# Kernel optimization log

Measured on AMD Instinct MI355X. Metric: run time of the kernel, lower is better.

## Reference

```python
import jax, jax.numpy as jnp
import numpy as np

B, OBS_LEN, IN_DIM, H, PRED_LEN = 32768, 8, 2, 128, 12
PRIOR_STD = 0.1
DROPOUT = 0.1


def _uni(k, shape, fan):
    b = 1.0 / np.sqrt(fan)
    return jax.random.uniform(k, shape, jnp.float32, -b, b)


def setup_inputs() -> dict:
    key = jax.random.key(0)
    ks = jax.random.split(key, 16)
    inp = {"obs_seq": jax.random.normal(ks[0], (B, OBS_LEN, IN_DIM), jnp.float32)}
    # encoder nn.LSTM params (torch init: U(-1/sqrt(H), 1/sqrt(H)))
    inp["enc_wih0"] = _uni(ks[1], (4 * H, IN_DIM), H)
    inp["enc_whh0"] = _uni(ks[2], (4 * H, H), H)
    inp["enc_bih0"] = _uni(ks[3], (4 * H,), H)
    inp["enc_bhh0"] = _uni(ks[4], (4 * H,), H)
    inp["enc_wih1"] = _uni(ks[5], (4 * H, H), H)
    inp["enc_whh1"] = _uni(ks[6], (4 * H, H), H)
    inp["enc_bih1"] = _uni(ks[7], (4 * H,), H)
    inp["enc_bhh1"] = _uni(ks[8], (4 * H,), H)
    # Bayesian decoder cell: kaiming_uniform(a=sqrt(5)) -> U(-1/sqrt(fan_in), 1/sqrt(fan_in))
    inp["din_wmu"] = _uni(ks[9], (4 * H, IN_DIM), IN_DIM)
    inp["din_wrho"] = jnp.full((4 * H, IN_DIM), -3.0, jnp.float32)
    inp["din_bmu"] = jnp.zeros((4 * H,), jnp.float32)
    inp["din_brho"] = jnp.full((4 * H,), -3.0, jnp.float32)
    inp["dhid_wmu"] = _uni(ks[10], (4 * H, H), H)
    inp["dhid_wrho"] = jnp.full((4 * H, H), -3.0, jnp.float32)
    inp["dhid_bmu"] = jnp.zeros((4 * H,), jnp.float32)
    inp["dhid_brho"] = jnp.full((4 * H,), -3.0, jnp.float32)
    # Bayesian output layer hidden -> 4
    inp["out_wmu"] = _uni(ks[11], (4, H), H)
    inp["out_wrho"] = jnp.full((4, H), -3.0, jnp.float32)
    inp["out_bmu"] = jnp.zeros((4,), jnp.float32)
    inp["out_brho"] = jnp.full((4,), -3.0, jnp.float32)
    return inp


def _lstm_layer(xs, wih, whh, bih, bhh):
    # xs: (B, T, D). PyTorch gate order: i, f, g, o.
    h0 = jnp.zeros((xs.shape[0], H), xs.dtype)
    bias = bih + bhh

    def step(carry, xt):
        h, c = carry
        g = xt @ wih.T + h @ whh.T + bias
        i, f, gg, o = jnp.split(g, 4, axis=-1)
        c = jax.nn.sigmoid(f) * c + jax.nn.sigmoid(i) * jnp.tanh(gg)
        h = jax.nn.sigmoid(o) * jnp.tanh(c)
        return (h, c), h

    (h, c), hs = jax.lax.scan(step, (h0, h0), jnp.swapaxes(xs, 0, 1))
    return jnp.swapaxes(hs, 0, 1), (h, c)


def _kl(mu, rho):
    # KL(N(mu, std^2) || N(0, PRIOR_STD^2)), std = softplus(rho)
    std = jax.nn.softplus(rho)
    return jnp.sum(jnp.log(PRIOR_STD / std) + (std * std + mu * mu) / (2.0 * PRIOR_STD * PRIOR_STD) - 0.5)


def _forward(obs_seq, enc_wih0, enc_whh0, enc_bih0, enc_bhh0,
             enc_wih1, enc_whh1, enc_bih1, enc_bhh1,
             din_wmu, din_wrho, din_bmu, din_brho,
             dhid_wmu, dhid_wrho, dhid_bmu, dhid_brho,
             out_wmu, out_wrho, out_bmu, out_brho):
    # ---- encoder (training mode: inter-layer dropout) ----
    hs0, _ = _lstm_layer(obs_seq, enc_wih0, enc_whh0, enc_bih0, enc_bhh0)
    keep = jax.random.bernoulli(jax.random.key(1), 1.0 - DROPOUT, hs0.shape)
    hs0 = jnp.where(keep, hs0 / (1.0 - DROPOUT), 0.0)
    _, (h, c) = _lstm_layer(hs0, enc_wih1, enc_whh1, enc_bih1, enc_bhh1)

    # ---- variational decoder: resample Bayesian weights every step ----
    din_wstd = jax.nn.softplus(din_wrho)
    din_bstd = jax.nn.softplus(din_brho)
    dhid_wstd = jax.nn.softplus(dhid_wrho)
    dhid_bstd = jax.nn.softplus(dhid_brho)
    out_wstd = jax.nn.softplus(out_wrho)
    out_bstd = jax.nn.softplus(out_brho)

    step_keys = jax.random.split(jax.random.key(2), PRED_LEN)

    def dstep(carry, k):
        h, c, x = carry
        k1, k2, k3, k4, k5, k6 = jax.random.split(k, 6)
        w_in = din_wmu + din_wstd * jax.random.normal(k1, din_wmu.shape, jnp.float32)
        b_in = din_bmu + din_bstd * jax.random.normal(k2, din_bmu.shape, jnp.float32)
        w_hid = dhid_wmu + dhid_wstd * jax.random.normal(k3, dhid_wmu.shape, jnp.float32)
        b_hid = dhid_bmu + dhid_bstd * jax.random.normal(k4, dhid_bmu.shape, jnp.float32)
        w_out = out_wmu + out_wstd * jax.random.normal(k5, out_wmu.shape, jnp.float32)
        b_out = out_bmu + out_bstd * jax.random.normal(k6, out_bmu.shape, jnp.float32)
        g = x @ w_in.T + h @ w_hid.T + (b_in + b_hid)
        i, f, gg, o = jnp.split(g, 4, axis=-1)
        c_new = jax.nn.sigmoid(f) * c + jax.nn.sigmoid(i) * jnp.tanh(gg)
        h_new = jax.nn.sigmoid(o) * jnp.tanh(c_new)
        out = h_new @ w_out.T + b_out
        mu_xy = out[:, :2]
        log_sigma = jnp.clip(out[:, 2:], -4.0, 2.0)
        return (h_new, c_new, mu_xy), (mu_xy, log_sigma)

    _, (mus, lss) = jax.lax.scan(dstep, (h, c, obs_seq[:, -1, :]), step_keys)
    mu = jnp.swapaxes(mus, 0, 1)        # (B, pred_len, 2)
    log_sigma = jnp.swapaxes(lss, 0, 1)  # (B, pred_len, 2)

    # KL is overwritten each step; since std/mu are eps-independent it equals the analytic sum
    kl = (_kl(din_wmu, din_wrho) + _kl(din_bmu, din_brho)
          + _kl(dhid_wmu, dhid_wrho) + _kl(dhid_bmu, dhid_brho)
          + _kl(out_wmu, out_wrho) + _kl(out_bmu, out_brho))
    return mu, log_sigma, kl


def reference(obs_seq, enc_wih0, enc_whh0, enc_bih0, enc_bhh0,
              enc_wih1, enc_whh1, enc_bih1, enc_bhh1,
              din_wmu, din_wrho, din_bmu, din_brho,
              dhid_wmu, dhid_wrho, dhid_bmu, dhid_brho,
              out_wmu, out_wrho, out_bmu, out_brho):
    return _forward(obs_seq, enc_wih0, enc_whh0, enc_bih0, enc_bhh0,
                    enc_wih1, enc_whh1, enc_bih1, enc_bhh1,
                    din_wmu, din_wrho, din_bmu, din_brho,
                    dhid_wmu, dhid_wrho, dhid_bmu, dhid_brho,
                    out_wmu, out_wrho, out_bmu, out_brho)
```

## Files before the change

kernel.cpp:

```cpp
#include <hip/hip_runtime.h>

typedef float f32x4 __attribute__((ext_vector_type(4)));
typedef float f32x2 __attribute__((ext_vector_type(2)));
typedef short bf16x8 __attribute__((ext_vector_type(8)));
typedef unsigned short ushort_t;
typedef unsigned int uint_t;

#define LOG2E  1.442695041f
#define LOG2E2 2.885390082f

__device__ __forceinline__ unsigned rotl32(unsigned x, unsigned r){ return (x << r) | (x >> (32u - r)); }

__device__ __forceinline__ void tf2x32(unsigned k0, unsigned k1, unsigned c0, unsigned c1,
                                       unsigned &o0, unsigned &o1){
  unsigned ks2 = k0 ^ k1 ^ 0x1BD11BDAu;
  unsigned x0 = c0 + k0, x1 = c1 + k1;
#define TFR(r) { x0 += x1; x1 = rotl32(x1, r); x1 ^= x0; }
  TFR(13) TFR(15) TFR(26) TFR(6)
  x0 += k1;  x1 += ks2 + 1u;
  TFR(17) TFR(29) TFR(16) TFR(24)
  x0 += ks2; x1 += k0 + 2u;
  TFR(13) TFR(15) TFR(26) TFR(6)
  x0 += k0;  x1 += k1 + 3u;
  TFR(17) TFR(29) TFR(16) TFR(24)
  x0 += k1;  x1 += ks2 + 4u;
  TFR(13) TFR(15) TFR(26) TFR(6)
  x0 += ks2; x1 += k0 + 5u;
#undef TFR
  o0 = x0; o1 = x1;
}

__device__ __forceinline__ float bits_to_u01(unsigned bits){
  return __uint_as_float((bits >> 9) | 0x3f800000u) - 1.0f;
}

__device__ __forceinline__ float erfinv_f(float x){
  float w = -log1pf(-x * x);
  float p;
  if (w < 5.0f){
    w -= 2.5f;
    p = 2.81022636e-08f;
    p = 3.43273939e-07f + p * w;
    p = -3.5233877e-06f + p * w;
    p = -4.39150654e-06f + p * w;
    p = 0.00021858087f + p * w;
    p = -0.00125372503f + p * w;
    p = -0.00417768164f + p * w;
    p = 0.246640727f + p * w;
    p = 1.50140941f + p * w;
  } else {
    w = sqrtf(w) - 3.0f;
    p = -0.000200214257f;
    p = 0.000100950558f + p * w;
    p = 0.00134934322f + p * w;
    p = -0.00367342844f + p * w;
    p = 0.00573950773f + p * w;
    p = -0.0076224613f + p * w;
    p = 0.00943887047f + p * w;
    p = 1.00167406f + p * w;
    p = 2.83297682f + p * w;
  }
  return p * x;
}

__device__ __forceinline__ ushort_t f2bf(float f){
  unsigned u = __float_as_uint(f);
  unsigned r = u + 0x7fffu + ((u >> 16) & 1u);
  return (ushort_t)(r >> 16);
}

__device__ __forceinline__ float norm_draw(unsigned sk0, unsigned sk1, unsigned g, unsigned e){
  unsigned gk0, gk1, b0, b1;
  tf2x32(sk0, sk1, 0u, g, gk0, gk1);
  tf2x32(gk0, gk1, 0u, e, b0, b1);
  unsigned bits = b0 ^ b1;
  float u01 = bits_to_u01(bits);
  const float LO = __uint_as_float(0xBF7FFFFFu);
  float u = u01 * 2.0f + LO;
  u = fmaxf(LO, u);
  return 1.41421356237f * erfinv_f(u);
}

__device__ __forceinline__ float softplus_f(float r){ return log1pf(expf(r)); }
__device__ __forceinline__ float gscale(int gate){ return gate == 2 ? LOG2E2 : LOG2E; }

__device__ __forceinline__ float fexp2(float x){
  float r;
  asm("v_exp_f32 %0, %1" : "=v"(r) : "v"(x));
  return r;
}
__device__ __forceinline__ float frcp(float x){ return __builtin_amdgcn_rcpf(x); }

__device__ __forceinline__ float lstm_act(float gi, float gf, float gg, float go, float& c){
  float Ef = fexp2(gf);
  float sf = Ef * frcp(1.0f + Ef);
  float EiN = fexp2(-gi);
  float Eg  = fexp2(gg);
  float cn = sf * c + (Eg - 1.0f) * frcp((1.0f + EiN) * (Eg + 1.0f));
  c = cn;
  float EoN = fexp2(-go);
  float Ec  = fexp2(cn * LOG2E2);
  return (Ec - 1.0f) * frcp((1.0f + EoN) * (Ec + 1.0f));
}

__device__ __forceinline__ float cp_lo(unsigned w){ return __uint_as_float(w << 16); }
__device__ __forceinline__ float cp_hi(unsigned w){ return __uint_as_float(w & 0xFFFF0000u); }
__device__ __forceinline__ unsigned cp_pack(float lo, float hi){
  return (__float_as_uint(hi) & 0xFFFF0000u) | (__float_as_uint(lo) >> 16);
}

constexpr int P0 = 136;
constexpr int P1 = 264;

__global__ void prep_all(
    const float* __restrict__ wih0,  const float* __restrict__ whh0,
    const float* __restrict__ bih0,  const float* __restrict__ bhh0,
    const float* __restrict__ wih1,  const float* __restrict__ whh1,
    const float* __restrict__ bih1,  const float* __restrict__ bhh1,
    const float* __restrict__ din_wmu, const float* __restrict__ din_wrho,
    const float* __restrict__ din_bmu, const float* __restrict__ din_brho,
    const float* __restrict__ dhid_wmu, const float* __restrict__ dhid_wrho,
    const float* __restrict__ dhid_bmu, const float* __restrict__ dhid_brho,
    const float* __restrict__ out_wmu, const float* __restrict__ out_wrho,
    const float* __restrict__ out_bmu, const float* __restrict__ out_brho,
    ushort_t* __restrict__ whh0b, ushort_t* __restrict__ w1e,
    float* __restrict__ wx0s, float* __restrict__ b0s, float* __restrict__ b1s,
    ushort_t* __restrict__ dwhidb, float* __restrict__ dwinb, float* __restrict__ dbsum,
    ushort_t* __restrict__ dwoutb, float* __restrict__ dbout,
    unsigned* __restrict__ maskT, float* __restrict__ out){
  const int blk = blockIdx.x, tid = threadIdx.x;

  if (blk < 4096){
    unsigned w = blk * 256u + tid;
    unsigned t = w >> 17, h = (w >> 10) & 127u, bw = w & 1023u;
    unsigned word = 0;
    #pragma unroll 4
    for (int i = 0; i < 32; ++i){
      unsigned ctr = (bw * 32u + i) * 1024u + t * 128u + h;
      unsigned o0, o1;
      tf2x32(0u, 1u, 0u, ctr, o0, o1);
      float u = bits_to_u01(o0 ^ o1);
      word |= (u < 0.9f ? 1u : 0u) << i;
    }
    maskT[w] = word;
  } else if (blk < 4872){
    int idx = (blk - 4096) * 256 + tid;
    if (idx < 65536){
      int row = idx >> 7;
      whh0b[idx] = f2bf(whh0[idx] * gscale(row >> 7));
    } else if (idx < 196608){
      int j = idx - 65536;
      int row = j >> 8, col = j & 255;
      float v = col < 128 ? whh1[row * 128 + col] : wih1[row * 128 + (col - 128)];
      w1e[j] = f2bf(v * gscale(row >> 7));
    } else if (idx < 197632){
      int j = idx - 196608;
      wx0s[j] = wih0[j] * gscale(j >> 8);
    } else if (idx < 198144){
      int j = idx - 197632;
      b0s[j] = (bih0[j] + bhh0[j]) * gscale(j >> 7);
    } else {
      int j = idx - 198144;
      b1s[j] = (bih1[j] + bhh1[j]) * gscale(j >> 7);
    }
  } else if (blk < 8113){
    int idx = (blk - 4872) * 256 + tid;
    if (idx < 829488){
      int s = idx / 69124, r = idx - s * 69124;
      unsigned sk0, sk1;
      tf2x32(0u, 2u, 0u, (unsigned)s, sk0, sk1);
      if (r < 65536){
        int row = r >> 7;
        float v = dhid_wmu[r] + softplus_f(dhid_wrho[r]) * norm_draw(sk0, sk1, 2u, (unsigned)r);
        dwhidb[s * 65536 + r] = f2bf(v * gscale(row >> 7));
      } else if (r < 66560){
        int j = r - 65536;
        float v = din_wmu[j] + softplus_f(din_wrho[j]) * norm_draw(sk0, sk1, 0u, (unsigned)j);
        dwinb[s * 1024 + j] = v * gscale(j >> 8);
      } else if (r < 67072){
        int j = r - 66560;
        float v1 = din_bmu[j]  + softplus_f(din_brho[j])  * norm_draw(sk0, sk1, 1u, (unsigned)j);
        float v2 = dhid_bmu[j] + softplus_f(dhid_brho[j]) * norm_draw(sk0, sk1, 3u, (unsigned)j);
        dbsum[s * 512 + j] = (v1 + v2) * gscale(j >> 7);
      } else if (r < 69120){
        int j = r - 67072;
        ushort_t v = 0;
        if (j < 512)
          v = f2bf(out_wmu[j] + softplus_f(out_wrho[j]) * norm_draw(sk0, sk1, 4u, (unsigned)j));
        dwoutb[s * 2048 + j] = v;
      } else {
        int j = r - 69120;
        dbout[s * 4 + j] = out_bmu[j] + softplus_f(out_brho[j]) * norm_draw(sk0, sk1, 5u, (unsigned)j);
      }
    }
  } else {
    int idx = (blk - 8113) * 256 + tid;
    float s = 0.f;
    if (idx < 68100){
      float mu, rho;
      if (idx < 1024){ mu = din_wmu[idx]; rho = din_wrho[idx]; }
      else if (idx < 1536){ mu = din_bmu[idx-1024]; rho = din_brho[idx-1024]; }
      else if (idx < 67072){ mu = dhid_wmu[idx-1536]; rho = dhid_wrho[idx-1536]; }
      else if (idx < 67584){ mu = dhid_bmu[idx-67072]; rho = dhid_brho[idx-67072]; }
      else if (idx < 68096){ mu = out_wmu[idx-67584]; rho = out_wrho[idx-67584]; }
      else { mu = out_bmu[idx-68096]; rho = out_brho[idx-68096]; }
      float stdv = softplus_f(rho);
      s = logf(0.1f / stdv) + (stdv * stdv + mu * mu) * 50.0f - 0.5f;
    }
    __shared__ float red[256];
    red[tid] = s;
    __syncthreads();
    for (int off = 128; off > 0; off >>= 1){
      if (tid < off) red[tid] += red[tid + off];
      __syncthreads();
    }
    if (tid == 0) atomicAdd(out + 1572864, red[0]);
  }
}

template<int NKI>
__device__ __forceinline__ void loadBfull(const ushort_t* __restrict__ W, int WROW,
                                          int hj, int lg, bf16x8 (&B)[4][NKI]){
  const ushort_t* wp = W + (size_t)hj * WROW + 8 * lg;
  #pragma unroll
  for (int g = 0; g < 4; ++g)
    #pragma unroll
    for (int ki = 0; ki < NKI; ++ki)
      B[g][ki] = *(const bf16x8*)(wp + (size_t)(128 * g) * WROW + 32 * ki);
}

#define ZACC(acc) { _Pragma("unroll") for (int g_=0;g_<4;++g_) _Pragma("unroll") for (int m_=0;m_<4;++m_) acc[g_][m_] = (f32x4){0.f,0.f,0.f,0.f}; }

template<int H, int NKI, int P>
__device__ __forceinline__ void gemm_half(const ushort_t* __restrict__ Hl, int lx, int lg,
                                          const bf16x8 (&B)[4][NKI], f32x4 (&acc)[4][4]){
  ZACC(acc);
  #pragma unroll
  for (int m = 0; m < 4; ++m){
    const ushort_t* hp = Hl + (64 * H + 16 * m + lx) * P + 8 * lg;
    bf16x8 a[NKI];
    #pragma unroll
    for (int ki = 0; ki < NKI; ++ki) a[ki] = *(const bf16x8*)(hp + 32 * ki);
    #pragma unroll
    for (int ki = 0; ki < NKI; ++ki)
      #pragma unroll
      for (int g = 0; g < 4; ++g)
        acc[g][m] = __builtin_amdgcn_mfma_f32_16x16x32_bf16(a[ki], B[g][ki], acc[g][m], 0, 0, 0);
  }
}

__device__ __forceinline__ void loadBchunk(const ushort_t* __restrict__ w1e, int hj, int lg,
                                           int kc, bf16x8 (&B)[4][2]){
  const ushort_t* wp = w1e + (size_t)hj * 256 + 64 * kc + 8 * lg;
  #pragma unroll
  for (int g = 0; g < 4; ++g){
    B[g][0] = *(const bf16x8*)(wp + (size_t)(128 * g) * 256);
    B[g][1] = *(const bf16x8*)(wp + (size_t)(128 * g) * 256 + 32);
  }
}

template<int H>
__device__ __forceinline__ void gemm1_half(const ushort_t* __restrict__ H1, int lx, int lg, int hj,
                                           const ushort_t* __restrict__ w1e,
                                           bf16x8 (&Bp)[4][2], bf16x8 (&Bq)[4][2], f32x4 (&acc)[4][4]){
  ZACC(acc);
  #pragma unroll
  for (int kc = 0; kc < 4; ++kc){
    bf16x8 (&cur)[4][2] = (kc & 1) ? Bq : Bp;
    bf16x8 (&nxt)[4][2] = (kc & 1) ? Bp : Bq;
    if (kc < 3) loadBchunk(w1e, hj, lg, kc + 1, nxt);
    #pragma unroll
    for (int m = 0; m < 4; ++m){
      const ushort_t* hp = H1 + (64 * H + 16 * m + lx) * P1 + 64 * kc + 8 * lg;
      bf16x8 a0 = *(const bf16x8*)(hp);
      bf16x8 a1 = *(const bf16x8*)(hp + 32);
      #pragma unroll
      for (int g = 0; g < 4; ++g)
        acc[g][m] = __builtin_amdgcn_mfma_f32_16x16x32_bf16(a0, cur[g][0], acc[g][m], 0, 0, 0);
      #pragma unroll
      for (int g = 0; g < 4; ++g)
        acc[g][m] = __builtin_amdgcn_mfma_f32_16x16x32_bf16(a1, cur[g][1], acc[g][m], 0, 0, 0);
    }
  }
}

template<int H>
__device__ __forceinline__ void pw0_half(int t, f32x4 (&acc)[4][4], unsigned* c0p,
    const float (&bv)[4], const float (&wav)[4], const float (&wbv)[4], uint4 mk,
    ushort_t* __restrict__ H0, ushort_t* __restrict__ H1, const float* __restrict__ OBSs,
    int hj, int lg){
  #pragma unroll
  for (int m = 0; m < 4; ++m){
    unsigned cwA = c0p[H*8 + m*2], cwB = c0p[H*8 + m*2 + 1];
    float cf0 = cp_lo(cwA), cf1 = cp_hi(cwA), cf2 = cp_lo(cwB), cf3 = cp_hi(cwB);
    const int wsel = H*2 + (m >> 1);
    unsigned mkw = wsel == 0 ? mk.x : wsel == 1 ? mk.y : wsel == 2 ? mk.z : mk.w;
    #pragma unroll
    for (int e = 0; e < 4; ++e){
      float& cf = e == 0 ? cf0 : e == 1 ? cf1 : e == 2 ? cf2 : cf3;
      int row = 64*H + 16*m + 4*lg + e;
      f32x2 xv = *(const f32x2*)(OBSs + row * 16 + 2 * t);
      float gi = acc[0][m][e] + bv[0] + xv.x * wav[0] + xv.y * wbv[0];
      float gf = acc[1][m][e] + bv[1] + xv.x * wav[1] + xv.y * wbv[1];
      float gg = acc[2][m][e] + bv[2] + xv.x * wav[2] + xv.y * wbv[2];
      float go = acc[3][m][e] + bv[3] + xv.x * wav[3] + xv.y * wbv[3];
      float hv = lstm_act(gi, gf, gg, go, cf);
      H0[row * P0 + hj] = f2bf(hv);
      unsigned keep = (mkw >> (((m & 1) << 4) + 4 * lg + e)) & 1u;
      H1[row * P1 + 128 + hj] = keep ? f2bf(hv * (1.0f / 0.9f)) : (ushort_t)0;
    }
    c0p[H*8 + m*2]     = cp_pack(cf0, cf1);
    c0p[H*8 + m*2 + 1] = cp_pack(cf2, cf3);
  }
}

template<int H>
__device__ __forceinline__ void pw1_half(f32x4 (&acc)[4][4], unsigned* c1p,
    const float (&bv)[4], ushort_t* __restrict__ H1, int hj, int lg){
  #pragma unroll
  for (int m = 0; m < 4; ++m){
    unsigned cwA = c1p[H*8 + m*2], cwB = c1p[H*8 + m*2 + 1];
    float cf0 = cp_lo(cwA), cf1 = cp_hi(cwA), cf2 = cp_lo(cwB), cf3 = cp_hi(cwB);
    #pragma unroll
    for (int e = 0; e < 4; ++e){
      float& cf = e == 0 ? cf0 : e == 1 ? cf1 : e == 2 ? cf2 : cf3;
      int row = 64*H + 16*m + 4*lg + e;
      float gi = acc[0][m][e] + bv[0];
      float gf = acc[1][m][e] + bv[1];
      float gg = acc[2][m][e] + bv[2];
      float go = acc[3][m][e] + bv[3];
      float hv = lstm_act(gi, gf, gg, go, cf);
      H1[row * P1 + hj] = f2bf(hv);
    }
    c1p[H*8 + m*2]     = cp_pack(cf0, cf1);
    c1p[H*8 + m*2 + 1] = cp_pack(cf2, cf3);
  }
}

template<int H>
__device__ __forceinline__ void pwd_half(f32x4 (&acc)[4][4], unsigned* c1p,
    const float (&bv)[4], const float (&wav)[4], const float (&wbv)[4],
    ushort_t* __restrict__ H1, const float* __restrict__ XDs, int hj, int lg){
  #pragma unroll
  for (int m = 0; m < 4; ++m){
    unsigned cwA = c1p[H*8 + m*2], cwB = c1p[H*8 + m*2 + 1];
    float cf0 = cp_lo(cwA), cf1 = cp_hi(cwA), cf2 = cp_lo(cwB), cf3 = cp_hi(cwB);
    #pragma unroll
    for (int e = 0; e < 4; ++e){
      float& cf = e == 0 ? cf0 : e == 1 ? cf1 : e == 2 ? cf2 : cf3;
      int row = 64*H + 16*m + 4*lg + e;
      f32x2 xv = *(const f32x2*)(XDs + 2 * row);
      float gi = acc[0][m][e] + bv[0] + xv.x * wav[0] + xv.y * wbv[0];
      float gf = acc[1][m][e] + bv[1] + xv.x * wav[1] + xv.y * wbv[1];
      float gg = acc[2][m][e] + bv[2] + xv.x * wav[2] + xv.y * wbv[2];
      float go = acc[3][m][e] + bv[3] + xv.x * wav[3] + xv.y * wbv[3];
      float hv = lstm_act(gi, gf, gg, go, cf);
      H1[row * P1 + hj] = f2bf(hv);
    }
    c1p[H*8 + m*2]     = cp_pack(cf0, cf1);
    c1p[H*8 + m*2 + 1] = cp_pack(cf2, cf3);
  }
}

__device__ __forceinline__ void out_head(int s, int mt, int lx, int lg, int b0,
    const ushort_t* __restrict__ H1, const ushort_t* __restrict__ dwoutb,
    const float* __restrict__ dbout, float* __restrict__ XDs, float* __restrict__ out){
  const ushort_t* wp = dwoutb + (size_t)s * 2048 + lx * 128 + 8 * lg;
  bf16x8 B0v = *(const bf16x8*)(wp);
  bf16x8 B1v = *(const bf16x8*)(wp + 32);
  bf16x8 B2v = *(const bf16x8*)(wp + 64);
  bf16x8 B3v = *(const bf16x8*)(wp + 96);
  const ushort_t* hp = H1 + (16 * mt + lx) * P1 + 8 * lg;
  f32x4 accO = {0.f, 0.f, 0.f, 0.f};
  accO = __builtin_amdgcn_mfma_f32_16x16x32_bf16(*(const bf16x8*)(hp),      B0v, accO, 0, 0, 0);
  accO = __builtin_amdgcn_mfma_f32_16x16x32_bf16(*(const bf16x8*)(hp + 32), B1v, accO, 0, 0, 0);
  accO = __builtin_amdgcn_mfma_f32_16x16x32_bf16(*(const bf16x8*)(hp + 64), B2v, accO, 0, 0, 0);
  accO = __builtin_amdgcn_mfma_f32_16x16x32_bf16(*(const bf16x8*)(hp + 96), B3v, accO, 0, 0, 0);
  if (lx < 4){
    float bo = dbout[s * 4 + lx];
    #pragma unroll
    for (int e = 0; e < 4; ++e){
      int row = 16 * mt + 4 * lg + e;
      float v = accO[e] + bo;
      int gb = b0 + row;
      if (lx < 2){
        out[gb * 24 + s * 2 + lx] = v;
        XDs[2 * row + lx] = v;
      } else {
        out[786432 + gb * 24 + s * 2 + (lx - 2)] = fminf(fmaxf(v, -4.0f), 2.0f);
      }
    }
  }
}

__global__ __launch_bounds__(512, 1) void lstm_main(
    const float* __restrict__ obs,
    const ushort_t* __restrict__ whh0b,
    const ushort_t* __restrict__ w1e,
    const float* __restrict__ wx0s,
    const float* __restrict__ b0s,
    const float* __restrict__ b1s,
    const ushort_t* __restrict__ dwhidb,
    const float* __restrict__ dwinb,
    const float* __restrict__ dbsum,
    const ushort_t* __restrict__ dwoutb,
    const float* __restrict__ dbout,
    const unsigned* __restrict__ maskT,
    float* __restrict__ out){
  __shared__ __align__(16) ushort_t H0s[128 * P0];
  __shared__ __align__(16) ushort_t H1s[128 * P1];
  __shared__ __align__(16) float OBSs[128 * 16];
  __shared__ float XDs[256];

  const int tid = threadIdx.x;
  const int wv = tid >> 6, l = tid & 63, lx = l & 15, lg = l >> 4;
  const int hj = 16 * wv + lx;
  const int b0 = blockIdx.x * 128;

  ((f32x4*)OBSs)[tid] = ((const f32x4*)(obs + (size_t)b0 * 16))[tid];
  {
    uint_t* p = (uint_t*)H0s;
    #pragma unroll 1
    for (int i = tid; i < 128 * P0 / 2; i += 512) p[i] = 0;
    uint_t* q = (uint_t*)H1s;
    #pragma unroll 1
    for (int i = tid; i < 128 * P1 / 2; i += 512) q[i] = 0;
  }

  float b0sv[4], wa0v[4], wb0v[4], b1sv[4];
  #pragma unroll
  for (int g = 0; g < 4; ++g){
    int j = 128 * g + hj;
    b0sv[g] = b0s[j];
    f32x2 w = *(const f32x2*)(wx0s + 2 * j);
    wa0v[g] = w.x; wb0v[g] = w.y;
    b1sv[g] = b1s[j];
  }
  unsigned c0p[16], c1p[16];
  #pragma unroll
  for (int i = 0; i < 16; ++i){ c0p[i] = 0; c1p[i] = 0; }

  f32x4 acc[4][4];
  bf16x8 Bf[4][4], Bp[4][2], Bq[4][2];

  __syncthreads();

  #pragma unroll 1
  for (int t = 0; t < 8; ++t){
    loadBfull<4>(whh0b, 128, hj, lg, Bf);
    const uint4 mk = *(const uint4*)(maskT + (size_t)t * 131072 + (size_t)hj * 1024 + blockIdx.x * 4);
    if (t > 0) pw1_half<1>(acc, c1p, b1sv, H1s, hj, lg);
    gemm_half<0, 4, P0>(H0s, lx, lg, Bf, acc);
    __syncthreads();
    pw0_half<0>(t, acc, c0p, b0sv, wa0v, wb0v, mk, H0s, H1s, OBSs, hj, lg);
    gemm_half<1, 4, P0>(H0s, lx, lg, Bf, acc);
    __syncthreads();
    loadBchunk(w1e, hj, lg, 0, Bp);
    pw0_half<1>(t, acc, c0p, b0sv, wa0v, wb0v, mk, H0s, H1s, OBSs, hj, lg);
    gemm1_half<0>(H1s, lx, lg, hj, w1e, Bp, Bq, acc);
    __syncthreads();
    loadBchunk(w1e, hj, lg, 0, Bp);
    pw1_half<0>(acc, c1p, b1sv, H1s, hj, lg);
    gemm1_half<1>(H1s, lx, lg, hj, w1e, Bp, Bq, acc);
    __syncthreads();
  }

  loadBfull<4>(dwhidb, 128, hj, lg, Bf);
  pw1_half<1>(acc, c1p, b1sv, H1s, hj, lg);
  gemm_half<0, 4, P1>(H1s, lx, lg, Bf, acc);
  if (tid < 256) XDs[tid] = OBSs[(tid >> 1) * 16 + 14 + (tid & 1)];
  __syncthreads();

  #pragma unroll 1
  for (int s = 0; s < 12; ++s){
    float bdv[4], wdx[4], wdy[4];
    #pragma unroll
    for (int g = 0; g < 4; ++g){
      int j = 128 * g + hj;
      bdv[g] = dbsum[s * 512 + j];
      f32x2 w = *(const f32x2*)(dwinb + 2 * (s * 512 + j));
      wdx[g] = w.x; wdy[g] = w.y;
    }
    pwd_half<0>(acc, c1p, bdv, wdx, wdy, H1s, XDs, hj, lg);
    gemm_half<1, 4, P1>(H1s, lx, lg, Bf, acc);
    if (s > 0 && wv >= 4) out_head(s - 1, wv, lx, lg, b0, H1s, dwoutb, dbout, XDs, out);
    __syncthreads();
    if (s < 11){
      loadBfull<4>(dwhidb + (size_t)(s + 1) * 65536, 128, hj, lg, Bf);
      pwd_half<1>(acc, c1p, bdv, wdx, wdy, H1s, XDs, hj, lg);
      gemm_half<0, 4, P1>(H1s, lx, lg, Bf, acc);
      if (wv < 4) out_head(s, wv, lx, lg, b0, H1s, dwoutb, dbout, XDs, out);
      __syncthreads();
    } else {
      pwd_half<1>(acc, c1p, bdv, wdx, wdy, H1s, XDs, hj, lg);
      if (wv < 4) out_head(11, wv, lx, lg, b0, H1s, dwoutb, dbout, XDs, out);
      __syncthreads();
      if (wv >= 4) out_head(11, wv, lx, lg, b0, H1s, dwoutb, dbout, XDs, out);
    }
  }
}

extern "C" void kernel_launch(void* const* d_in, const int* in_sizes, int n_in,
                              void* d_out, int out_size, void* d_ws, size_t ws_size,
                              hipStream_t stream){
  (void)in_sizes; (void)n_in; (void)out_size; (void)ws_size;
  const float* obs   = (const float*)d_in[0];
  const float* wih0  = (const float*)d_in[1];
  const float* whh0  = (const float*)d_in[2];
  const float* bih0  = (const float*)d_in[3];
  const float* bhh0  = (const float*)d_in[4];
  const float* wih1  = (const float*)d_in[5];
  const float* whh1  = (const float*)d_in[6];
  const float* bih1  = (const float*)d_in[7];
  const float* bhh1  = (const float*)d_in[8];
  const float* din_wmu  = (const float*)d_in[9];
  const float* din_wrho = (const float*)d_in[10];
  const float* din_bmu  = (const float*)d_in[11];
  const float* din_brho = (const float*)d_in[12];
  const float* dhid_wmu  = (const float*)d_in[13];
  const float* dhid_wrho = (const float*)d_in[14];
  const float* dhid_bmu  = (const float*)d_in[15];
  const float* dhid_brho = (const float*)d_in[16];
  const float* out_wmu  = (const float*)d_in[17];
  const float* out_wrho = (const float*)d_in[18];
  const float* out_bmu  = (const float*)d_in[19];
  const float* out_brho = (const float*)d_in[20];

  char* wsb = (char*)d_ws;
  ushort_t* whh0b  = (ushort_t*)(wsb + 0);
  ushort_t* w1e    = (ushort_t*)(wsb + 131072);
  float*    wx0s   = (float*)(wsb + 393216);
  float*    b0s    = (float*)(wsb + 397312);
  float*    b1s    = (float*)(wsb + 399360);
  ushort_t* dwhidb = (ushort_t*)(wsb + 401408);
  float*    dwinb  = (float*)(wsb + 1974272);
  float*    dbsum  = (float*)(wsb + 2023424);
  ushort_t* dwoutb = (ushort_t*)(wsb + 2048000);
  float*    dbout  = (float*)(wsb + 2097152);
  unsigned* maskT  = (unsigned*)(wsb + 2097344);

  hipMemsetAsync((float*)d_out + 1572864, 0, 4, stream);

  prep_all<<<8380, 256, 0, stream>>>(
      wih0, whh0, bih0, bhh0, wih1, whh1, bih1, bhh1,
      din_wmu, din_wrho, din_bmu, din_brho,
      dhid_wmu, dhid_wrho, dhid_bmu, dhid_brho,
      out_wmu, out_wrho, out_bmu, out_brho,
      whh0b, w1e, wx0s, b0s, b1s, dwhidb, dwinb, dbsum, dwoutb, dbout,
      maskT, (float*)d_out);

  lstm_main<<<256, 512, 0, stream>>>(obs, whh0b, w1e, wx0s, b0s, b1s,
                                     dwhidb, dwinb, dbsum, dwoutb, dbout,
                                     maskT, (float*)d_out);
}
```

Measured before the change: 958.6 us.

## Stream weight fragments per k-step and raise occupancy to two blocks per CU

Replaces the fully register-resident weight tiles (16 bf16x8 per thread) with a double-buffered per-k-step stream of 4 fragments, reloading from global/L2 inside each GEMM. Launch bounds change from 1 to 2 blocks per CU to cut register pressure. The dropout mask layout is also reordered so each block reads a contiguous region. The cost is repeated weight fetches every half-step instead of reuse across both halves; with only 256 blocks the extra occupancy may not be usable.

```diff
diff --git a/kernel.cpp b/kernel.cpp
--- a/kernel.cpp
+++ b/kernel.cpp
@@ -127,22 +127,22 @@
     float* __restrict__ wx0s, float* __restrict__ b0s, float* __restrict__ b1s,
     ushort_t* __restrict__ dwhidb, float* __restrict__ dwinb, float* __restrict__ dbsum,
     ushort_t* __restrict__ dwoutb, float* __restrict__ dbout,
-    unsigned* __restrict__ maskT, float* __restrict__ out){
+    unsigned* __restrict__ maskM, float* __restrict__ out){
   const int blk = blockIdx.x, tid = threadIdx.x;
 
   if (blk < 4096){
     unsigned w = blk * 256u + tid;
-    unsigned t = w >> 17, h = (w >> 10) & 127u, bw = w & 1023u;
+    unsigned mb = w >> 12, t = (w >> 9) & 7u, hj = (w >> 2) & 127u, bw = w & 3u;
     unsigned word = 0;
     #pragma unroll 4
     for (int i = 0; i < 32; ++i){
-      unsigned ctr = (bw * 32u + i) * 1024u + t * 128u + h;
+      unsigned ctr = (mb * 128u + bw * 32u + i) * 1024u + t * 128u + hj;
       unsigned o0, o1;
       tf2x32(0u, 1u, 0u, ctr, o0, o1);
       float u = bits_to_u01(o0 ^ o1);
       word |= (u < 0.9f ? 1u : 0u) << i;
     }
-    maskT[w] = word;
+    maskM[w] = word;
   } else if (blk < 4872){
     int idx = (blk - 4096) * 256 + tid;
     if (idx < 65536){
@@ -218,68 +218,70 @@
   }
 }
 
-template<int NKI>
-__device__ __forceinline__ void loadBfull(const ushort_t* __restrict__ W, int WROW,
-                                          int hj, int lg, bf16x8 (&B)[4][NKI]){
+__device__ __forceinline__ void preB(const ushort_t* __restrict__ W, int WROW,
+                                     int hj, int lg, bf16x8 (&B)[4]){
   const ushort_t* wp = W + (size_t)hj * WROW + 8 * lg;
   #pragma unroll
   for (int g = 0; g < 4; ++g)
-    #pragma unroll
-    for (int ki = 0; ki < NKI; ++ki)
-      B[g][ki] = *(const bf16x8*)(wp + (size_t)(128 * g) * WROW + 32 * ki);
+    B[g] = *(const bf16x8*)(wp + (size_t)(128 * g) * WROW);
 }
 
 #define ZACC(acc) { _Pragma("unroll") for (int g_=0;g_<4;++g_) _Pragma("unroll") for (int m_=0;m_<4;++m_) acc[g_][m_] = (f32x4){0.f,0.f,0.f,0.f}; }
 
-template<int H, int NKI, int P>
-__device__ __forceinline__ void gemm_half(const ushort_t* __restrict__ Hl, int lx, int lg,
-                                          const bf16x8 (&B)[4][NKI], f32x4 (&acc)[4][4]){
+template<int H, int P>
+__device__ __forceinline__ void gemm_w128(const ushort_t* __restrict__ Hl,
+                                          const ushort_t* __restrict__ W,
+                                          int lx, int lg, int hj,
+                                          f32x4 (&acc)[4][4], bf16x8 (&Bc)[4]){
   ZACC(acc);
-  #pragma unroll
-  for (int m = 0; m < 4; ++m){
-    const ushort_t* hp = Hl + (64 * H + 16 * m + lx) * P + 8 * lg;
-    bf16x8 a[NKI];
-    #pragma unroll
-    for (int ki = 0; ki < NKI; ++ki) a[ki] = *(const bf16x8*)(hp + 32 * ki);
-    #pragma unroll
-    for (int ki = 0; ki < NKI; ++ki)
+  const ushort_t* wp = W + (size_t)hj * 128 + 8 * lg;
+  #pragma unroll
+  for (int ki = 0; ki < 4; ++ki){
+    bf16x8 Bn[4];
+    if (ki < 3){
       #pragma unroll
       for (int g = 0; g < 4; ++g)
-        acc[g][m] = __builtin_amdgcn_mfma_f32_16x16x32_bf16(a[ki], B[g][ki], acc[g][m], 0, 0, 0);
-  }
-}
-
-__device__ __forceinline__ void loadBchunk(const ushort_t* __restrict__ w1e, int hj, int lg,
-                                           int kc, bf16x8 (&B)[4][2]){
-  const ushort_t* wp = w1e + (size_t)hj * 256 + 64 * kc + 8 * lg;
-  #pragma unroll
-  for (int g = 0; g < 4; ++g){
-    B[g][0] = *(const bf16x8*)(wp + (size_t)(128 * g) * 256);
-    B[g][1] = *(const bf16x8*)(wp + (size_t)(128 * g) * 256 + 32);
-  }
-}
-
-template<int H>
-__device__ __forceinline__ void gemm1_half(const ushort_t* __restrict__ H1, int lx, int lg, int hj,
-                                           const ushort_t* __restrict__ w1e,
-                                           bf16x8 (&Bp)[4][2], bf16x8 (&Bq)[4][2], f32x4 (&acc)[4][4]){
-  ZACC(acc);
-  #pragma unroll
-  for (int kc = 0; kc < 4; ++kc){
-    bf16x8 (&cur)[4][2] = (kc & 1) ? Bq : Bp;
-    bf16x8 (&nxt)[4][2] = (kc & 1) ? Bp : Bq;
-    if (kc < 3) loadBchunk(w1e, hj, lg, kc + 1, nxt);
+        Bn[g] = *(const bf16x8*)(wp + (size_t)(128 * g) * 128 + 32 * (ki + 1));
+    }
     #pragma unroll
     for (int m = 0; m < 4; ++m){
-      const ushort_t* hp = H1 + (64 * H + 16 * m + lx) * P1 + 64 * kc + 8 * lg;
-      bf16x8 a0 = *(const bf16x8*)(hp);
-      bf16x8 a1 = *(const bf16x8*)(hp + 32);
+      bf16x8 a = *(const bf16x8*)(Hl + (64 * H + 16 * m + lx) * P + 32 * ki + 8 * lg);
       #pragma unroll
       for (int g = 0; g < 4; ++g)
-        acc[g][m] = __builtin_amdgcn_mfma_f32_16x16x32_bf16(a0, cur[g][0], acc[g][m], 0, 0, 0);
+        acc[g][m] = __builtin_amdgcn_mfma_f32_16x16x32_bf16(a, Bc[g], acc[g][m], 0, 0, 0);
+    }
+    if (ki < 3){
+      #pragma unroll
+      for (int g = 0; g < 4; ++g) Bc[g] = Bn[g];
+    }
+  }
+}
+
+template<int H>
+__device__ __forceinline__ void gemm_w256(const ushort_t* __restrict__ H1,
+                                          const ushort_t* __restrict__ W,
+                                          int lx, int lg, int hj,
+                                          f32x4 (&acc)[4][4], bf16x8 (&Bc)[4]){
+  ZACC(acc);
+  const ushort_t* wp = W + (size_t)hj * 256 + 8 * lg;
+  #pragma unroll
+  for (int ki = 0; ki < 8; ++ki){
+    bf16x8 Bn[4];
+    if (ki < 7){
       #pragma unroll
       for (int g = 0; g < 4; ++g)
-        acc[g][m] = __builtin_amdgcn_mfma_f32_16x16x32_bf16(a1, cur[g][1], acc[g][m], 0, 0, 0);
+        Bn[g] = *(const bf16x8*)(wp + (size_t)(128 * g) * 256 + 32 * (ki + 1));
+    }
+    #pragma unroll
+    for (int m = 0; m < 4; ++m){
+      bf16x8 a = *(const bf16x8*)(H1 + (64 * H + 16 * m + lx) * P1 + 32 * ki + 8 * lg);
+      #pragma unroll
+      for (int g = 0; g < 4; ++g)
+        acc[g][m] = __builtin_amdgcn_mfma_f32_16x16x32_bf16(a, Bc[g], acc[g][m], 0, 0, 0);
+    }
+    if (ki < 7){
+      #pragma unroll
+      for (int g = 0; g < 4; ++g) Bc[g] = Bn[g];
     }
   }
 }
@@ -366,16 +368,12 @@
     const ushort_t* __restrict__ H1, const ushort_t* __restrict__ dwoutb,
     const float* __restrict__ dbout, float* __restrict__ XDs, float* __restrict__ out){
   const ushort_t* wp = dwoutb + (size_t)s * 2048 + lx * 128 + 8 * lg;
-  bf16x8 B0v = *(const bf16x8*)(wp);
-  bf16x8 B1v = *(const bf16x8*)(wp + 32);
-  bf16x8 B2v = *(const bf16x8*)(wp + 64);
-  bf16x8 B3v = *(const bf16x8*)(wp + 96);
   const ushort_t* hp = H1 + (16 * mt + lx) * P1 + 8 * lg;
   f32x4 accO = {0.f, 0.f, 0.f, 0.f};
-  accO = __builtin_amdgcn_mfma_f32_16x16x32_bf16(*(const bf16x8*)(hp),      B0v, accO, 0, 0, 0);
-  accO = __builtin_amdgcn_mfma_f32_16x16x32_bf16(*(const bf16x8*)(hp + 32), B1v, accO, 0, 0, 0);
-  accO = __builtin_amdgcn_mfma_f32_16x16x32_bf16(*(const bf16x8*)(hp + 64), B2v, accO, 0, 0, 0);
-  accO = __builtin_amdgcn_mfma_f32_16x16x32_bf16(*(const bf16x8*)(hp + 96), B3v, accO, 0, 0, 0);
+  accO = __builtin_amdgcn_mfma_f32_16x16x32_bf16(*(const bf16x8*)(hp),      *(const bf16x8*)(wp),      accO, 0, 0, 0);
+  accO = __builtin_amdgcn_mfma_f32_16x16x32_bf16(*(const bf16x8*)(hp + 32), *(const bf16x8*)(wp + 32), accO, 0, 0, 0);
+  accO = __builtin_amdgcn_mfma_f32_16x16x32_bf16(*(const bf16x8*)(hp + 64), *(const bf16x8*)(wp + 64), accO, 0, 0, 0);
+  accO = __builtin_amdgcn_mfma_f32_16x16x32_bf16(*(const bf16x8*)(hp + 96), *(const bf16x8*)(wp + 96), accO, 0, 0, 0);
   if (lx < 4){
     float bo = dbout[s * 4 + lx];
     #pragma unroll
@@ -393,7 +391,7 @@
   }
 }
 
-__global__ __launch_bounds__(512, 1) void lstm_main(
+__global__ __launch_bounds__(512, 2) void lstm_main(
     const float* __restrict__ obs,
     const ushort_t* __restrict__ whh0b,
     const ushort_t* __restrict__ w1e,
@@ -405,7 +403,7 @@
     const float* __restrict__ dbsum,
     const ushort_t* __restrict__ dwoutb,
     const float* __restrict__ dbout,
-    const unsigned* __restrict__ maskT,
+    const unsigned* __restrict__ maskM,
     float* __restrict__ out){
   __shared__ __align__(16) ushort_t H0s[128 * P0];
   __shared__ __align__(16) ushort_t H1s[128 * P1];
@@ -441,38 +439,40 @@
   for (int i = 0; i < 16; ++i){ c0p[i] = 0; c1p[i] = 0; }
 
   f32x4 acc[4][4];
-  bf16x8 Bf[4][4], Bp[4][2], Bq[4][2];
+  bf16x8 Bc[4];
 
   __syncthreads();
 
   #pragma unroll 1
   for (int t = 0; t < 8; ++t){
-    loadBfull<4>(whh0b, 128, hj, lg, Bf);
-    const uint4 mk = *(const uint4*)(maskT + (size_t)t * 131072 + (size_t)hj * 1024 + blockIdx.x * 4);
+    preB(whh0b, 128, hj, lg, Bc);
+    const uint4 mk = *(const uint4*)(maskM + (size_t)blockIdx.x * 4096 + (size_t)t * 512 + (size_t)hj * 4);
     if (t > 0) pw1_half<1>(acc, c1p, b1sv, H1s, hj, lg);
-    gemm_half<0, 4, P0>(H0s, lx, lg, Bf, acc);
+    gemm_w128<0, P0>(H0s, whh0b, lx, lg, hj, acc, Bc);
     __syncthreads();
+    preB(whh0b, 128, hj, lg, Bc);
     pw0_half<0>(t, acc, c0p, b0sv, wa0v, wb0v, mk, H0s, H1s, OBSs, hj, lg);
-    gemm_half<1, 4, P0>(H0s, lx, lg, Bf, acc);
+    gemm_w128<1, P0>(H0s, whh0b, lx, lg, hj, acc, Bc);
     __syncthreads();
-    loadBchunk(w1e, hj, lg, 0, Bp);
+    preB(w1e, 256, hj, lg, Bc);
     pw0_half<1>(t, acc, c0p, b0sv, wa0v, wb0v, mk, H0s, H1s, OBSs, hj, lg);
-    gemm1_half<0>(H1s, lx, lg, hj, w1e, Bp, Bq, acc);
+    gemm_w256<0>(H1s, w1e, lx, lg, hj, acc, Bc);
     __syncthreads();
-    loadBchunk(w1e, hj, lg, 0, Bp);
+    preB(w1e, 256, hj, lg, Bc);
     pw1_half<0>(acc, c1p, b1sv, H1s, hj, lg);
-    gemm1_half<1>(H1s, lx, lg, hj, w1e, Bp, Bq, acc);
+    gemm_w256<1>(H1s, w1e, lx, lg, hj, acc, Bc);
     __syncthreads();
   }
 
-  loadBfull<4>(dwhidb, 128, hj, lg, Bf);
+  preB(dwhidb, 128, hj, lg, Bc);
   pw1_half<1>(acc, c1p, b1sv, H1s, hj, lg);
-  gemm_half<0, 4, P1>(H1s, lx, lg, Bf, acc);
+  gemm_w128<0, P1>(H1s, dwhidb, lx, lg, hj, acc, Bc);
   if (tid < 256) XDs[tid] = OBSs[(tid >> 1) * 16 + 14 + (tid & 1)];
   __syncthreads();
 
   #pragma unroll 1
   for (int s = 0; s < 12; ++s){
+    const ushort_t* dw_cur = dwhidb + (size_t)s * 65536;
     float bdv[4], wdx[4], wdy[4];
     #pragma unroll
     for (int g = 0; g < 4; ++g){
@@ -481,14 +481,16 @@
       f32x2 w = *(const f32x2*)(dwinb + 2 * (s * 512 + j));
       wdx[g] = w.x; wdy[g] = w.y;
     }
+    preB(dw_cur, 128, hj, lg, Bc);
     pwd_half<0>(acc, c1p, bdv, wdx, wdy, H1s, XDs, hj, lg);
-    gemm_half<1, 4, P1>(H1s, lx, lg, Bf, acc);
+    gemm_w128<1, P1>(H1s, dw_cur, lx, lg, hj, acc, Bc);
     if (s > 0 && wv >= 4) out_head(s - 1, wv, lx, lg, b0, H1s, dwoutb, dbout, XDs, out);
     __syncthreads();
     if (s < 11){
-      loadBfull<4>(dwhidb + (size_t)(s + 1) * 65536, 128, hj, lg, Bf);
+      const ushort_t* dw_next = dwhidb + (size_t)(s + 1) * 65536;
+      preB(dw_next, 128, hj, lg, Bc);
       pwd_half<1>(acc, c1p, bdv, wdx, wdy, H1s, XDs, hj, lg);
-      gemm_half<0, 4, P1>(H1s, lx, lg, Bf, acc);
+      gemm_w128<0, P1>(H1s, dw_next, lx, lg, hj, acc, Bc);
       if (wv < 4) out_head(s, wv, lx, lg, b0, H1s, dwoutb, dbout, XDs, out);
       __syncthreads();
     } else {
@@ -537,7 +539,7 @@
   float*    dbsum  = (float*)(wsb + 2023424);
   ushort_t* dwoutb = (ushort_t*)(wsb + 2048000);
   float*    dbout  = (float*)(wsb + 2097152);
-  unsigned* maskT  = (unsigned*)(wsb + 2097344);
+  unsigned* maskM  = (unsigned*)(wsb + 2097344);
 
   hipMemsetAsync((float*)d_out + 1572864, 0, 4, stream);
 
@@ -547,9 +549,9 @@
       dhid_wmu, dhid_wrho, dhid_bmu, dhid_brho,
       out_wmu, out_wrho, out_bmu, out_brho,
       whh0b, w1e, wx0s, b0s, b1s, dwhidb, dwinb, dbsum, dwoutb, dbout,
-      maskT, (float*)d_out);
+      maskM, (float*)d_out);
 
   lstm_main<<<256, 512, 0, stream>>>(obs, whh0b, w1e, wx0s, b0s, b1s,
                                      dwhidb, dwinb, dbsum, dwoutb, dbout,
-                                     maskT, (float*)d_out);
-}
+                                     maskM, (float*)d_out);
+}
```

After: 836.8 us. 1.15x faster.
